# Kernel optimization log

Measured on AMD Instinct MI355X. Metric: run time of the kernel, lower is better.

The kernel has to match this reference:

```python
import jax, jax.numpy as jnp
import numpy as np

D_MODEL = 1024
NUM_HEADS = 16
DEPTH = D_MODEL // NUM_HEADS
FF_DIM = 1024
MAX_POS = 2048
EPS = 1e-6


def positional_encoding(position, d_model):
    pos = np.arange(position)[:, None].astype(np.float32)
    i = np.arange(d_model)[None, :].astype(np.float32)
    angle_rates = 1.0 / np.power(10000.0, 2.0 * np.floor(i / 2.0) / np.float32(d_model))
    angle_rads = pos * angle_rates
    angle_rads[:, 0::2] = np.sin(angle_rads[:, 0::2])
    angle_rads[:, 1::2] = np.cos(angle_rads[:, 1::2])
    return jnp.asarray(angle_rads[None, ...], dtype=jnp.float32)  # [1, P, D]


def setup_inputs() -> dict:
    key = jax.random.key(0)
    ks = jax.random.split(key, 16)
    B, S, D, F = 4, 2048, D_MODEL, FF_DIM
    s = 1.0 / np.sqrt(D)
    inp = {
        "inputs": jax.random.normal(ks[0], (B, S, D), jnp.float32),
        "wq": jax.random.normal(ks[1], (D, D), jnp.float32) * s,
        "bq": jnp.zeros((D,), jnp.float32),
        "wk": jax.random.normal(ks[2], (D, D), jnp.float32) * s,
        "bk": jnp.zeros((D,), jnp.float32),
        "wv": jax.random.normal(ks[3], (D, D), jnp.float32) * s,
        "bv": jnp.zeros((D,), jnp.float32),
        "wo": jax.random.normal(ks[4], (D, D), jnp.float32) * s,
        "bo": jnp.zeros((D,), jnp.float32),
        "w1": jax.random.normal(ks[5], (D, F), jnp.float32) * s,
        "b1": jnp.zeros((F,), jnp.float32),
        "w2": jax.random.normal(ks[6], (F, F), jnp.float32) * (1.0 / np.sqrt(F)),
        "b2": jnp.zeros((F,), jnp.float32),
        "ln1_g": jnp.ones((D,), jnp.float32),
        "ln1_b": jnp.zeros((D,), jnp.float32),
        "ln2_g": jnp.ones((D,), jnp.float32),
        "ln2_b": jnp.zeros((D,), jnp.float32),
    }
    return inp


def layer_norm(x, g, b):
    mu = jnp.mean(x, axis=-1, keepdims=True)
    var = jnp.mean(jnp.square(x - mu), axis=-1, keepdims=True)
    return (x - mu) / jnp.sqrt(var + EPS) * g + b


def reference(inputs, wq, bq, wk, bk, wv, bv, wo, bo, w1, b1, w2, b2,
              ln1_g, ln1_b, ln2_g, ln2_b):
    B, S, D = inputs.shape
    pe = positional_encoding(MAX_POS, FF_DIM)[:, :S, :]
    x = inputs + pe

    def heads(t):  # [B,S,D] -> [B,H,S,depth]
        return t.reshape(B, S, NUM_HEADS, DEPTH).transpose(0, 2, 1, 3)

    q = heads(x @ wq + bq)
    k = heads(x @ wk + bk)
    v = heads(x @ wv + bv)

    logits = jnp.einsum("bhqd,bhkd->bhqk", q, k) / jnp.sqrt(jnp.float32(DEPTH))
    attn = jax.nn.softmax(logits, axis=-1)
    ctx = jnp.einsum("bhqk,bhkd->bhqd", attn, v)
    ctx = ctx.transpose(0, 2, 1, 3).reshape(B, S, D)
    attn_out = ctx @ wo + bo  # dropout is identity (inference)

    out1 = layer_norm(x + attn_out, ln1_g, ln1_b)
    ffn = jax.nn.relu(out1 @ w1 + b1) @ w2 + b2
    return layer_norm(out1 + ffn, ln2_g, ln2_b)
```

## Files before the change

### kernel.cpp

```cpp
#include <hip/hip_runtime.h>
#include <hip/hip_bf16.h>
#include <math.h>

typedef __bf16 bf16;
typedef __bf16 bf16x8 __attribute__((ext_vector_type(8)));
typedef __bf16 bf16x4 __attribute__((ext_vector_type(4)));
typedef float f32x4 __attribute__((ext_vector_type(4)));

#define MFMA16(A, B, C) __builtin_amdgcn_mfma_f32_16x16x32_bf16((A), (B), (C), 0, 0, 0)
#define GLD16(g, l)                                                        \
  __builtin_amdgcn_global_load_lds(                                        \
      (const __attribute__((address_space(1))) void*)(g),                  \
      (__attribute__((address_space(3))) void*)(l), 16, 0, 0)

__global__ __launch_bounds__(256) void k_xgen(const float* __restrict__ in,
                                              float* __restrict__ xf,
                                              bf16* __restrict__ xb) {
  int idx = (blockIdx.x * 256 + threadIdx.x) * 4;
  int d = idx & 1023;
  int s = (idx >> 10) & 2047;
  float4 v = *(const float4*)(in + idx);
  float r[4] = {v.x, v.y, v.z, v.w};
  float o[4];
#pragma unroll
  for (int j = 0; j < 4; ++j) {
    int dj = d + j;
    float fe = (float)(dj & ~1) * (1.0f / 1024.0f);
    float rate = exp2f(fe * -13.2877123795f);
    float ang = (float)s * rate;
    float pe = (dj & 1) ? cosf(ang) : sinf(ang);
    o[j] = r[j] + pe;
  }
  *(float4*)(xf + idx) = make_float4(o[0], o[1], o[2], o[3]);
  bf16x4 ob = {(bf16)o[0], (bf16)o[1], (bf16)o[2], (bf16)o[3]};
  *(bf16x4*)(xb + idx) = ob;
}

__global__ __launch_bounds__(256) void k_wt(const float* __restrict__ w,
                                            bf16* __restrict__ wt) {
  __shared__ float t[32][33];
  int tx = threadIdx.x & 31;
  int ty = threadIdx.x >> 5;
  int bk = blockIdx.y * 32;
  int bn = blockIdx.x * 32;
#pragma unroll
  for (int q = 0; q < 4; ++q) {
    int y = ty + q * 8;
    t[y][tx] = w[(size_t)(bk + y) * 1024 + bn + tx];
  }
  __syncthreads();
#pragma unroll
  for (int q = 0; q < 4; ++q) {
    int y = ty + q * 8;
    wt[(size_t)(bn + y) * 1024 + bk + tx] = (bf16)t[tx][y];
  }
}

enum { M_HEADS = 0, M_VT = 1, M_RESID = 2, M_RELU = 3 };

template <int MODE>
__global__ __launch_bounds__(256) void k_gemm(const bf16* __restrict__ A,
                                              const bf16* __restrict__ Bt,
                                              const float* __restrict__ bias,
                                              const float* __restrict__ resid,
                                              bf16* __restrict__ outb,
                                              float* __restrict__ outf) {
  __shared__ bf16 lA[128 * 32];
  __shared__ bf16 lB[128 * 32];
  const int t = threadIdx.x;
  const int l = t & 63;
  const int w = t >> 6;
  const int wm = w >> 1, wn = w & 1;
  const int tm = blockIdx.x * 128;
  const int tn = blockIdx.y * 128;
  const int lr = t >> 2;
  const int lc = (t & 3) * 8;
  const int g = l >> 4, c16 = l & 15;
  char* lAb = (char*)lA + w * 1024;
  char* lBb = (char*)lB + w * 1024;
  const bf16* a0 = A + (size_t)(tm + lr) * 1024 + lc;
  const bf16* a1 = A + (size_t)(tm + 64 + lr) * 1024 + lc;
  const bf16* b0 = Bt + (size_t)(tn + lr) * 1024 + lc;
  const bf16* b1 = Bt + (size_t)(tn + 64 + lr) * 1024 + lc;
  f32x4 acc[4][4] = {};
  for (int kb = 0; kb < 1024; kb += 32) {
    __syncthreads();
    GLD16(a0 + kb, lAb);
    GLD16(a1 + kb, lAb + 4096);
    GLD16(b0 + kb, lBb);
    GLD16(b1 + kb, lBb + 4096);
    __syncthreads();
    bf16x8 aF[4], bF[4];
#pragma unroll
    for (int i = 0; i < 4; ++i)
      aF[i] = *(const bf16x8*)&lA[(wm * 64 + i * 16 + c16) * 32 + g * 8];
#pragma unroll
    for (int j = 0; j < 4; ++j)
      bF[j] = *(const bf16x8*)&lB[(wn * 64 + j * 16 + c16) * 32 + g * 8];
#pragma unroll
    for (int i = 0; i < 4; ++i)
#pragma unroll
      for (int j = 0; j < 4; ++j)
        acc[i][j] = MFMA16(aF[i], bF[j], acc[i][j]);
  }
#pragma unroll
  for (int i = 0; i < 4; ++i) {
#pragma unroll
    for (int j = 0; j < 4; ++j) {
      int gc = tn + wn * 64 + j * 16 + c16;
      float bv = bias[gc];
#pragma unroll
      for (int r = 0; r < 4; ++r) {
        int gr = tm + wm * 64 + i * 16 + g * 4 + r;
        float v = acc[i][j][r] + bv;
        if (MODE == M_HEADS) {
          int b = gr >> 11, s = gr & 2047, h = gc >> 6, dd = gc & 63;
          outb[((size_t)(b * 16 + h) * 2048 + s) * 64 + dd] = (bf16)v;
        } else if (MODE == M_VT) {
          int b = gr >> 11, s = gr & 2047, h = gc >> 6, dd = gc & 63;
          outb[((size_t)(b * 16 + h) * 64 + dd) * 2048 + s] = (bf16)v;
        } else if (MODE == M_RESID) {
          size_t o = (size_t)gr * 1024 + gc;
          outf[o] = v + resid[o];
        } else {
          outb[(size_t)gr * 1024 + gc] = (bf16)fmaxf(v, 0.0f);
        }
      }
    }
  }
}

__global__ __launch_bounds__(256) void k_attn(const bf16* __restrict__ q,
                                              const bf16* __restrict__ k,
                                              const bf16* __restrict__ vt,
                                              bf16* __restrict__ ctx) {
  __shared__ bf16 Kl[4096];
  __shared__ bf16 Vl[4096];
  __shared__ bf16 Pl[4][1024];
  const int lin = blockIdx.x + (blockIdx.y << 5);
  const int swz = (lin & 7) * 256 + (lin >> 3);
  const int qt = swz & 31;
  const int bh = swz >> 5;
  const int t = threadIdx.x;
  const int w = t >> 6, l = t & 63;
  const int g = l >> 4, c16 = l & 15;
  const int qbase = qt * 64 + w * 16;
  const bf16* Qh = q + (size_t)bh * 2048 * 64;
  const bf16* Kh = k + (size_t)bh * 2048 * 64;
  const bf16* Vh = vt + (size_t)bh * 64 * 2048;

  bf16x8 aQ0, aQ1;
  {
    bf16x8 t0 = *(const bf16x8*)(Qh + (size_t)(qbase + c16) * 64 + g * 8);
    bf16x8 t1 = *(const bf16x8*)(Qh + (size_t)(qbase + c16) * 64 + 32 + g * 8);
#pragma unroll
    for (int j = 0; j < 8; ++j) {
      aQ0[j] = (bf16)((float)t0[j] * 0.18033688f);
      aQ1[j] = (bf16)((float)t1[j] * 0.18033688f);
    }
  }

  const int sr = l >> 2, ch = (l & 3) * 8;
  const int b0 = w, b1 = 4 + w;
  const bf16* ksrc0 = Kh + (size_t)((b0 >> 1) * 16 + sr) * 64 + (b0 & 1) * 32 + ch;
  const bf16* ksrc1 = Kh + (size_t)((b1 >> 1) * 16 + sr) * 64 + (b1 & 1) * 32 + ch;
  const bf16* vsrc0 = Vh + (size_t)((b0 >> 1) * 16 + sr) * 2048 + (b0 & 1) * 32 + ch;
  const bf16* vsrc1 = Vh + (size_t)((b1 >> 1) * 16 + sr) * 2048 + (b1 & 1) * 32 + ch;
  char* kdst0 = (char*)Kl + w * 1024;
  char* kdst1 = (char*)Kl + 4096 + w * 1024;
  char* vdst0 = (char*)Vl + w * 1024;
  char* vdst1 = (char*)Vl + 4096 + w * 1024;

  f32x4 acc[4] = {};
  float psum[4] = {0.0f, 0.0f, 0.0f, 0.0f};

  for (int kb = 0; kb < 2048; kb += 64) {
    __syncthreads();
    GLD16(ksrc0 + (size_t)kb * 64, kdst0);
    GLD16(ksrc1 + (size_t)kb * 64, kdst1);
    GLD16(vsrc0 + kb, vdst0);
    GLD16(vsrc1 + kb, vdst1);
    __syncthreads();

    f32x4 sv[4];
    const char* KB_ = (const char*)Kl;
#pragma unroll
    for (int s = 0; s < 4; ++s) {
      bf16x8 k0 = *(const bf16x8*)(KB_ + ((s * 2 + 0) * 16 + c16) * 64 + g * 16);
      bf16x8 k1 = *(const bf16x8*)(KB_ + ((s * 2 + 1) * 16 + c16) * 64 + g * 16);
      f32x4 z = {};
      z = MFMA16(aQ0, k0, z);
      z = MFMA16(aQ1, k1, z);
      sv[s] = z;
    }

    bf16* pw = &Pl[w][0];
#pragma unroll
    for (int r = 0; r < 4; ++r) {
      float p0 = exp2f(sv[0][r]);
      float p1 = exp2f(sv[1][r]);
      float p2 = exp2f(sv[2][r]);
      float p3 = exp2f(sv[3][r]);
      psum[r] += (p0 + p1) + (p2 + p3);
      int q4 = (g * 4 + r) * 32;
      pw[q4 + c16]            = (bf16)p0;
      pw[q4 + 16 + c16]       = (bf16)p1;
      pw[512 + q4 + c16]      = (bf16)p2;
      pw[512 + q4 + 16 + c16] = (bf16)p3;
    }

    asm volatile("s_waitcnt lgkmcnt(0)" ::: "memory");

    const char* VB_ = (const char*)Vl;
    const char* PB_ = (const char*)&Pl[w][0];
#pragma unroll
    for (int ks = 0; ks < 2; ++ks) {
      bf16x8 aP = *(const bf16x8*)(PB_ + (ks * 16 + c16) * 64 + g * 16);
#pragma unroll
      for (int c = 0; c < 4; ++c) {
        bf16x8 bV = *(const bf16x8*)(VB_ + ((c * 2 + ks) * 16 + c16) * 64 + g * 16);
        acc[c] = MFMA16(aP, bV, acc[c]);
      }
    }
  }

  const int b = bh >> 4, h = bh & 15;
#pragma unroll
  for (int r = 0; r < 4; ++r) {
    float ts = psum[r];
    ts += __shfl_xor(ts, 1);
    ts += __shfl_xor(ts, 2);
    ts += __shfl_xor(ts, 4);
    ts += __shfl_xor(ts, 8);
    float inv = 1.0f / ts;
    int srow = qbase + g * 4 + r;
#pragma unroll
    for (int c = 0; c < 4; ++c) {
      ctx[(size_t)(b * 2048 + srow) * 1024 + h * 64 + c * 16 + c16] =
          (bf16)(acc[c][r] * inv);
    }
  }
}

template <bool WRITE_F32, bool WRITE_BF16>
__global__ __launch_bounds__(256) void k_ln(const float* __restrict__ x,
                                            const float* __restrict__ gamma,
                                            const float* __restrict__ beta,
                                            float* __restrict__ outf,
                                            bf16* __restrict__ outb) {
  const int row = blockIdx.x;
  const int t = threadIdx.x;
  const float* xr = x + (size_t)row * 1024;
  float4 v = *(const float4*)(xr + t * 4);
  float s = v.x + v.y + v.z + v.w;
  float s2 = v.x * v.x + v.y * v.y + v.z * v.z + v.w * v.w;
#pragma unroll
  for (int off = 1; off < 64; off <<= 1) {
    s += __shfl_xor(s, off);
    s2 += __shfl_xor(s2, off);
  }
  __shared__ float ps[4], ps2[4];
  int wv = t >> 6, l = t & 63;
  if (l == 0) { ps[wv] = s; ps2[wv] = s2; }
  __syncthreads();
  s = ps[0] + ps[1] + ps[2] + ps[3];
  s2 = ps2[0] + ps2[1] + ps2[2] + ps2[3];
  float mu = s * (1.0f / 1024.0f);
  float var = s2 * (1.0f / 1024.0f) - mu * mu;
  float rstd = rsqrtf(var + 1e-6f);
  float4 gv = *(const float4*)(gamma + t * 4);
  float4 bv = *(const float4*)(beta + t * 4);
  float y0 = (v.x - mu) * rstd * gv.x + bv.x;
  float y1 = (v.y - mu) * rstd * gv.y + bv.y;
  float y2 = (v.z - mu) * rstd * gv.z + bv.z;
  float y3 = (v.w - mu) * rstd * gv.w + bv.w;
  if (WRITE_F32)
    *(float4*)(outf + (size_t)row * 1024 + t * 4) = make_float4(y0, y1, y2, y3);
  if (WRITE_BF16) {
    bf16x4 ob = {(bf16)y0, (bf16)y1, (bf16)y2, (bf16)y3};
    *(bf16x4*)(outb + (size_t)row * 1024 + t * 4) = ob;
  }
}

extern "C" void kernel_launch(void* const* d_in, const int* in_sizes, int n_in,
                              void* d_out, int out_size, void* d_ws, size_t ws_size,
                              hipStream_t stream) {
  const float* in   = (const float*)d_in[0];
  const float* wq   = (const float*)d_in[1];
  const float* bq   = (const float*)d_in[2];
  const float* wk   = (const float*)d_in[3];
  const float* bk   = (const float*)d_in[4];
  const float* wv   = (const float*)d_in[5];
  const float* bv   = (const float*)d_in[6];
  const float* wo   = (const float*)d_in[7];
  const float* bo   = (const float*)d_in[8];
  const float* w1   = (const float*)d_in[9];
  const float* b1   = (const float*)d_in[10];
  const float* w2   = (const float*)d_in[11];
  const float* b2   = (const float*)d_in[12];
  const float* ln1g = (const float*)d_in[13];
  const float* ln1b = (const float*)d_in[14];
  const float* ln2g = (const float*)d_in[15];
  const float* ln2b = (const float*)d_in[16];

  uint8_t* W = (uint8_t*)d_ws;
  const size_t WSZ = (size_t)1024 * 1024 * 2;
  bf16* wtq = (bf16*)(W + 0 * WSZ);
  bf16* wtk = (bf16*)(W + 1 * WSZ);
  bf16* wtv = (bf16*)(W + 2 * WSZ);
  bf16* wto = (bf16*)(W + 3 * WSZ);
  bf16* wt1 = (bf16*)(W + 4 * WSZ);
  bf16* wt2 = (bf16*)(W + 5 * WSZ);
  const size_t XF_OFF  = 6 * WSZ;
  const size_t F32SZ   = (size_t)8192 * 1024 * 4;
  const size_t BF16SZ  = (size_t)8192 * 1024 * 2;
  float* XF  = (float*)(W + XF_OFF);
  const size_t XB_OFF  = XF_OFF + F32SZ;
  bf16* XB   = (bf16*)(W + XB_OFF);
  const size_t QB_OFF  = XB_OFF + BF16SZ;
  bf16* QB   = (bf16*)(W + QB_OFF);
  const size_t KB_OFF  = QB_OFF + BF16SZ;
  bf16* KB   = (bf16*)(W + KB_OFF);
  const size_t VT_OFF  = KB_OFF + BF16SZ;
  bf16* VT   = (bf16*)(W + VT_OFF);
  const size_t CTX_OFF = VT_OFF + BF16SZ;
  bf16* CTX  = (bf16*)(W + CTX_OFF);
  float* S1   = (float*)(W + XB_OFF);
  float* O1F  = (float*)(W + KB_OFF);
  bf16*  O1B  = (bf16*)(W + CTX_OFF);
  bf16*  HB   = (bf16*)(W + XF_OFF);
  float* S2   = (float*)(W + XB_OFF);
  float* OUT  = (float*)d_out;

  k_xgen<<<8192, 256, 0, stream>>>(in, XF, XB);
  dim3 tg(32, 32);
  k_wt<<<tg, 256, 0, stream>>>(wq, wtq);
  k_wt<<<tg, 256, 0, stream>>>(wk, wtk);
  k_wt<<<tg, 256, 0, stream>>>(wv, wtv);
  k_wt<<<tg, 256, 0, stream>>>(wo, wto);
  k_wt<<<tg, 256, 0, stream>>>(w1, wt1);
  k_wt<<<tg, 256, 0, stream>>>(w2, wt2);

  dim3 gg(64, 8);
  k_gemm<M_HEADS><<<gg, 256, 0, stream>>>(XB, wtq, bq, nullptr, QB, nullptr);
  k_gemm<M_HEADS><<<gg, 256, 0, stream>>>(XB, wtk, bk, nullptr, KB, nullptr);
  k_gemm<M_VT><<<gg, 256, 0, stream>>>(XB, wtv, bv, nullptr, VT, nullptr);

  k_attn<<<dim3(32, 64), 256, 0, stream>>>(QB, KB, VT, CTX);

  k_gemm<M_RESID><<<gg, 256, 0, stream>>>(CTX, wto, bo, XF, nullptr, S1);
  k_ln<true, true><<<8192, 256, 0, stream>>>(S1, ln1g, ln1b, O1F, O1B);
  k_gemm<M_RELU><<<gg, 256, 0, stream>>>(O1B, wt1, b1, nullptr, HB, nullptr);
  k_gemm<M_RESID><<<gg, 256, 0, stream>>>(HB, wt2, b2, O1F, nullptr, S2);
  k_ln<true, false><<<8192, 256, 0, stream>>>(S2, ln2g, ln2b, OUT, nullptr);
}
```

Measured before the change: 474.3 us.

## Fuse Q/K/V projections into one GEMM and swizzle P tile in LDS

Combines the three Q, K and V projection GEMMs into a single launch over a 3072-wide output. Each column segment picks its bias and output layout: head-major for Q and K, transposed for V. This depends on wtq/wtk/wtv and QB/KB/VT being laid out contiguously in the workspace. Separately, the attention kernel's softmax-probability LDS tile is XOR-swizzled on write and read to reduce bank conflicts. The aim is fewer launches, a larger grid for better occupancy, and cheaper LDS traffic.

```diff
diff --git a/kernel.cpp b/kernel.cpp
--- a/kernel.cpp
+++ b/kernel.cpp
@@ -56,7 +56,7 @@
   }
 }
 
-enum { M_HEADS = 0, M_VT = 1, M_RESID = 2, M_RELU = 3 };
+enum { M_HEADS = 0, M_VT = 1, M_RESID = 2, M_RELU = 3, M_QKV = 4 };
 
 template <int MODE>
 __global__ __launch_bounds__(256) void k_gemm(const bf16* __restrict__ A,
@@ -108,12 +108,27 @@
 #pragma unroll
     for (int j = 0; j < 4; ++j) {
       int gc = tn + wn * 64 + j * 16 + c16;
-      float bv = bias[gc];
+      float bv;
+      if (MODE == M_QKV) {
+        int seg = gc >> 10;
+        const float* bp = seg == 0 ? bias : (seg == 1 ? resid : (const float*)outf);
+        bv = bp[gc & 1023];
+      } else {
+        bv = bias[gc];
+      }
 #pragma unroll
       for (int r = 0; r < 4; ++r) {
         int gr = tm + wm * 64 + i * 16 + g * 4 + r;
         float v = acc[i][j][r] + bv;
-        if (MODE == M_HEADS) {
+        if (MODE == M_QKV) {
+          int seg = gc >> 10, col = gc & 1023;
+          int b = gr >> 11, s = gr & 2047, h = col >> 6, dd = col & 63;
+          bf16* dst = outb + (size_t)seg * (8192ull * 1024);
+          if (seg < 2)
+            dst[((size_t)(b * 16 + h) * 2048 + s) * 64 + dd] = (bf16)v;
+          else
+            dst[((size_t)(b * 16 + h) * 64 + dd) * 2048 + s] = (bf16)v;
+        } else if (MODE == M_HEADS) {
           int b = gr >> 11, s = gr & 2047, h = gc >> 6, dd = gc & 63;
           outb[((size_t)(b * 16 + h) * 2048 + s) * 64 + dd] = (bf16)v;
         } else if (MODE == M_VT) {
@@ -171,6 +186,11 @@
   char* vdst0 = (char*)Vl + w * 1024;
   char* vdst1 = (char*)Vl + 4096 + w * 1024;
 
+  const int c8v = c16 & 7;
+  const int e0 = (((c16 >> 3) ^ g) & 3) * 8 + c8v;
+  const int e1 = ((((c16 >> 3) | 2) ^ g) & 3) * 8 + c8v;
+  const int rdch = ((g ^ (c16 >> 2)) & 3) * 16;
+
   f32x4 acc[4] = {};
   float psum[4] = {0.0f, 0.0f, 0.0f, 0.0f};
 
@@ -202,11 +222,11 @@
       float p2 = exp2f(sv[2][r]);
       float p3 = exp2f(sv[3][r]);
       psum[r] += (p0 + p1) + (p2 + p3);
-      int q4 = (g * 4 + r) * 32;
-      pw[q4 + c16]            = (bf16)p0;
-      pw[q4 + 16 + c16]       = (bf16)p1;
-      pw[512 + q4 + c16]      = (bf16)p2;
-      pw[512 + q4 + 16 + c16] = (bf16)p3;
+      int q32 = (g * 4 + r) * 32;
+      pw[q32 + e0]       = (bf16)p0;
+      pw[q32 + e1]       = (bf16)p1;
+      pw[512 + q32 + e0] = (bf16)p2;
+      pw[512 + q32 + e1] = (bf16)p3;
     }
 
     asm volatile("s_waitcnt lgkmcnt(0)" ::: "memory");
@@ -215,7 +235,7 @@
     const char* PB_ = (const char*)&Pl[w][0];
 #pragma unroll
     for (int ks = 0; ks < 2; ++ks) {
-      bf16x8 aP = *(const bf16x8*)(PB_ + (ks * 16 + c16) * 64 + g * 16);
+      bf16x8 aP = *(const bf16x8*)(PB_ + ks * 1024 + c16 * 64 + rdch);
 #pragma unroll
       for (int c = 0; c < 4; ++c) {
         bf16x8 bV = *(const bf16x8*)(VB_ + ((c * 2 + ks) * 16 + c16) * 64 + g * 16);
@@ -341,13 +361,11 @@
   k_wt<<<tg, 256, 0, stream>>>(w1, wt1);
   k_wt<<<tg, 256, 0, stream>>>(w2, wt2);
 
+  k_gemm<M_QKV><<<dim3(64, 24), 256, 0, stream>>>(XB, wtq, bq, bk, QB, (float*)bv);
+
+  k_attn<<<dim3(32, 64), 256, 0, stream>>>(QB, KB, VT, CTX);
+
   dim3 gg(64, 8);
-  k_gemm<M_HEADS><<<gg, 256, 0, stream>>>(XB, wtq, bq, nullptr, QB, nullptr);
-  k_gemm<M_HEADS><<<gg, 256, 0, stream>>>(XB, wtk, bk, nullptr, KB, nullptr);
-  k_gemm<M_VT><<<gg, 256, 0, stream>>>(XB, wtv, bv, nullptr, VT, nullptr);
-
-  k_attn<<<dim3(32, 64), 256, 0, stream>>>(QB, KB, VT, CTX);
-
   k_gemm<M_RESID><<<gg, 256, 0, stream>>>(CTX, wto, bo, XF, nullptr, S1);
   k_ln<true, true><<<8192, 256, 0, stream>>>(S1, ln1g, ln1b, O1F, O1B);
   k_gemm<M_RELU><<<gg, 256, 0, stream>>>(O1B, wt1, b1, nullptr, HB, nullptr);
```

After: 469.8 us. No clear change (-1.0%).
